# Performance work log

Hardware: AMD Instinct MI355X
Metric: run time of the kernel (lower is better)

## Reference

```python
import jax, jax.numpy as jnp
import numpy as np

N = 50000      # nodes
E = 800000     # edges
DIN = 128      # input_dim
FN = 128       # filter_num
OUT = 16       # out_dim (classes)
K = 10         # APPNP power-iteration steps
ALPHA = 0.1    # teleport probability


def _glorot_linear(key, fan_in, fan_out):
    s = 1.0 / np.sqrt(fan_in)
    kw, kb = jax.random.split(key)
    W = jax.random.uniform(kw, (fan_in, fan_out), jnp.float32, -s, s)
    b = jax.random.uniform(kb, (fan_out,), jnp.float32, -s, s)
    return W, b


def setup_inputs() -> dict:
    key = jax.random.key(0)
    ks = jax.random.split(key, 6)
    x = jax.random.normal(ks[0], (N, DIN), jnp.float32)
    edge_index = jax.random.randint(ks[1], (2, E), 0, N, dtype=jnp.int64)
    W1, b1 = _glorot_linear(ks[2], DIN, FN)
    W2, b2 = _glorot_linear(ks[3], FN, FN)
    W3, b3 = _glorot_linear(ks[4], FN, FN)
    Wc, bc = _glorot_linear(ks[5], FN, OUT)  # Conv1d kernel_size=1 == per-node linear
    return {"x": x, "edge_index": edge_index, "W1": W1, "b1": b1,
            "W2": W2, "b2": b2, "W3": W3, "b3": b3, "Wc": Wc, "bc": bc}


def _appnp(x, row, col, w, n):
    # x_{k+1} = (1-alpha) * A_hat @ x_k + alpha * x_0
    h = x
    def step(xk, _):
        msg = w[:, None] * xk[row]                      # [E+N, F] gather
        agg = jax.ops.segment_sum(msg, col, num_segments=n)  # scatter-add SpMM
        return (1.0 - ALPHA) * agg + ALPHA * h, None
    out, _ = jax.lax.scan(step, x, None, length=K)
    return out


def reference(x, edge_index, W1, b1, W2, b2, W3, b3, Wc, bc):
    n = x.shape[0]
    # gcn_norm with self-loops: w_e = deg(col)^-1/2 * deg(row)^-1/2
    loops = jnp.arange(n, dtype=edge_index.dtype)
    row = jnp.concatenate([edge_index[0], loops])
    col = jnp.concatenate([edge_index[1], loops])
    deg = jax.ops.segment_sum(jnp.ones_like(col, x.dtype), col, num_segments=n)
    dinv = jnp.where(deg > 0, jax.lax.rsqrt(deg), 0.0)
    w = dinv[row] * dinv[col]

    h = jax.nn.relu(_appnp(x @ W1 + b1, row, col, w, n))
    h = jax.nn.relu(_appnp(h @ W2 + b2, row, col, w, n))
    h = jax.nn.relu(_appnp(h @ W3 + b3, row, col, w, n))
    logits = h @ Wc + bc                                # 1x1 Conv1d == linear
    return jax.nn.log_softmax(logits, axis=1)
```

## Files before the change

kernel.cpp:

```cpp
#include <hip/hip_runtime.h>
#include <math.h>

#define FD 128
#define NOUT 16
#define ALPHA_F 0.1f

typedef short short8 __attribute__((ext_vector_type(8)));
typedef float f32x4 __attribute__((ext_vector_type(4)));

__device__ __forceinline__ float bflo(unsigned u) { return __uint_as_float(u << 16); }
__device__ __forceinline__ float bfhi(unsigned u) { return __uint_as_float(u & 0xffff0000u); }
__device__ __forceinline__ unsigned f2bf(float f) {
    unsigned u = __float_as_uint(f);
    u += 0x7fffu + ((u >> 16) & 1u);
    return u >> 16;
}
__device__ __forceinline__ unsigned pack2(float a, float b) {
    return f2bf(a) | (f2bf(b) << 16);
}


__global__ void count_kernel(const int* __restrict__ cols, int* __restrict__ cnt, int e) {
    int i = blockIdx.x * blockDim.x + threadIdx.x;
    if (i < e) atomicAdd(&cnt[cols[i]], 1);
}

__global__ void dinv_kernel(const int* __restrict__ cnt, float* __restrict__ dinv, int n) {
    int i = blockIdx.x * blockDim.x + threadIdx.x;
    if (i < n) dinv[i] = rsqrtf((float)(cnt[i] + 1));
}

__device__ __forceinline__ int padded(int cnt) { return (cnt + 8) & ~7; }

__global__ void scan_partial_kernel(const int* __restrict__ cnt, int* __restrict__ bsum, int n) {
    __shared__ int sh[256];
    int base = blockIdx.x * 1024 + threadIdx.x * 4;
    int s = 0;
    #pragma unroll
    for (int j = 0; j < 4; ++j) { int i = base + j; if (i < n) s += padded(cnt[i]); }
    sh[threadIdx.x] = s; __syncthreads();
    for (int d = 128; d > 0; d >>= 1) {
        if ((int)threadIdx.x < d) sh[threadIdx.x] += sh[threadIdx.x + d];
        __syncthreads();
    }
    if (threadIdx.x == 0) bsum[blockIdx.x] = sh[0];
}

__global__ void scan_base_kernel(int* __restrict__ bsum, int* __restrict__ off, int nb, int n) {
    if (threadIdx.x == 0 && blockIdx.x == 0) {
        int run = 0;
        for (int b = 0; b < nb; ++b) { int t = bsum[b]; bsum[b] = run; run += t; }
        off[n] = run;
    }
}

__global__ void scan_final_kernel(const int* __restrict__ cnt, const int* __restrict__ bsum,
                                  int* __restrict__ off, int* __restrict__ cur, int n) {
    __shared__ int sh[256];
    int t = threadIdx.x;
    int base_i = blockIdx.x * 1024 + t * 4;
    int v[4]; int s = 0;
    #pragma unroll
    for (int j = 0; j < 4; ++j) { int i = base_i + j; v[j] = (i < n) ? padded(cnt[i]) : 0; s += v[j]; }
    sh[t] = s; __syncthreads();
    for (int d = 1; d < 256; d <<= 1) {
        int x = (t >= d) ? sh[t - d] : 0;
        __syncthreads();
        sh[t] += x;
        __syncthreads();
    }
    int excl = sh[t] - s + bsum[blockIdx.x];
    #pragma unroll
    for (int j = 0; j < 4; ++j) {
        int i = base_i + j;
        if (i < n) { off[i] = excl; cur[i] = excl; }
        excl += v[j];
    }
}

__global__ void fill_edges_kernel(const int* __restrict__ rows, const int* __restrict__ cols,
                                  const float* __restrict__ dinv, int* __restrict__ cur,
                                  unsigned* __restrict__ eg, int e) {
    int i = blockIdx.x * blockDim.x + threadIdx.x;
    if (i < e) {
        int r = rows[i];
        int c = cols[i];
        int pos = atomicAdd(&cur[c], 1);
        eg[pos] = (f2bf(dinv[r] * dinv[c]) << 16) | (unsigned)r;
    }
}

__global__ void fill_loops_kernel(const float* __restrict__ dinv, int* __restrict__ cur,
                                  unsigned* __restrict__ eg, int n) {
    int i = blockIdx.x * blockDim.x + threadIdx.x;
    if (i < n) {
        int pos = atomicAdd(&cur[i], 1);
        eg[pos] = (f2bf(dinv[i] * dinv[i]) << 16) | (unsigned)i;
    }
}


__global__ void wtrans_kernel(const float* __restrict__ W, unsigned* __restrict__ Wt) {
    int idx = blockIdx.x * 256 + threadIdx.x;
    if (idx < 128 * 64) {
        int c = idx >> 6, ku = idx & 63;
        Wt[idx] = pack2(W[(2 * ku) * FD + c], W[(2 * ku + 1) * FD + c]);
    }
}

__global__ void xconv_kernel(const float* __restrict__ x, unsigned* __restrict__ Xb, int total) {
    int idx = blockIdx.x * blockDim.x + threadIdx.x;
    if (idx < total) {
        float2 f = ((const float2*)x)[idx];
        Xb[idx] = pack2(f.x, f.y);
    }
}

__global__ __launch_bounds__(256, 4)
void gemm_mfma_kernel(const unsigned* __restrict__ Xb, const unsigned* __restrict__ Wt,
                      const float* __restrict__ bias,
                      unsigned* __restrict__ Ab, unsigned* __restrict__ Z0b, int n) {
    int l = threadIdx.x & 63;
    int w = threadIdx.x >> 6;
    int l15 = l & 15, lq = l >> 4;
    int r0 = blockIdx.x * 64 + w * 16;
    int arow = min(r0 + l15, n - 1);
    const unsigned* aptr = Xb + (size_t)arow * 64 + lq * 4;
    const unsigned* bptr = Wt + (size_t)l15 * 64 + lq * 4;

    f32x4 acc[8];
    #pragma unroll
    for (int nt = 0; nt < 8; ++nt) acc[nt] = (f32x4){0.f, 0.f, 0.f, 0.f};

    #pragma unroll
    for (int kk = 0; kk < 4; ++kk) {
        short8 af = *(const short8*)(aptr + kk * 16);
        #pragma unroll
        for (int nt = 0; nt < 8; ++nt) {
            short8 bf = *(const short8*)(bptr + nt * 1024 + kk * 16);
            acc[nt] = __builtin_amdgcn_mfma_f32_16x16x32_bf16(af, bf, acc[nt], 0, 0, 0);
        }
    }

    #pragma unroll
    for (int nt = 0; nt < 8; ++nt) {
        float b_ = bias[nt * 16 + l15];
        #pragma unroll
        for (int j = 0; j < 4; ++j) {
            float v = acc[nt][j] + b_;
            float vp = __shfl_xor(v, 1);
            int row = r0 + lq * 4 + j;
            if (!(l & 1) && row < n) {
                int cu = nt * 8 + (l15 >> 1);
                Ab[(size_t)row * 64 + cu]  = pack2(v, vp);
                Z0b[(size_t)row * 64 + cu] = pack2(ALPHA_F * v, ALPHA_F * vp);
            }
        }
    }
}

__global__ __launch_bounds__(256, 8)
void spmm_bf16_kernel(const int* __restrict__ off, const unsigned* __restrict__ eg,
                      const unsigned* __restrict__ Xin, const unsigned* __restrict__ X0b,
                      unsigned* __restrict__ Xout, int n, int relu) {
    int node = blockIdx.x * 8 + ((int)threadIdx.x >> 5);
    if (node >= n) return;
    int lane31 = threadIdx.x & 31;
    int s = off[node];
    int degpad = off[node + 1] - s;
    int dother = __shfl_xor(degpad, 32);
    int dm = max(degpad, dother);
    const uint2* Xg = (const uint2*)Xin;
    uint2 x0 = ((const uint2*)X0b)[node * 32 + lane31];
    float a0 = 0.f, a1 = 0.f, a2 = 0.f, a3 = 0.f;

    for (int base = 0; base < dm; base += 8) {
        int p = s + min(base, degpad - 8);
        bool live = base < degpad;
        uint4 ra = *(const uint4*)(eg + p);
        uint4 rb = *(const uint4*)(eg + p + 4);
        uint2 g0 = Xg[(ra.x & 0xffffu) * 32 + lane31];
        uint2 g1 = Xg[(ra.y & 0xffffu) * 32 + lane31];
        uint2 g2 = Xg[(ra.z & 0xffffu) * 32 + lane31];
        uint2 g3 = Xg[(ra.w & 0xffffu) * 32 + lane31];
        uint2 g4 = Xg[(rb.x & 0xffffu) * 32 + lane31];
        uint2 g5 = Xg[(rb.y & 0xffffu) * 32 + lane31];
        uint2 g6 = Xg[(rb.z & 0xffffu) * 32 + lane31];
        uint2 g7 = Xg[(rb.w & 0xffffu) * 32 + lane31];
        float w0 = live ? bfhi(ra.x) : 0.f;
        float w1 = live ? bfhi(ra.y) : 0.f;
        float w2 = live ? bfhi(ra.z) : 0.f;
        float w3 = live ? bfhi(ra.w) : 0.f;
        float w4 = live ? bfhi(rb.x) : 0.f;
        float w5 = live ? bfhi(rb.y) : 0.f;
        float w6 = live ? bfhi(rb.z) : 0.f;
        float w7 = live ? bfhi(rb.w) : 0.f;
        a0 += w0 * bflo(g0.x); a1 += w0 * bfhi(g0.x); a2 += w0 * bflo(g0.y); a3 += w0 * bfhi(g0.y);
        a0 += w1 * bflo(g1.x); a1 += w1 * bfhi(g1.x); a2 += w1 * bflo(g1.y); a3 += w1 * bfhi(g1.y);
        a0 += w2 * bflo(g2.x); a1 += w2 * bfhi(g2.x); a2 += w2 * bflo(g2.y); a3 += w2 * bfhi(g2.y);
        a0 += w3 * bflo(g3.x); a1 += w3 * bfhi(g3.x); a2 += w3 * bflo(g3.y); a3 += w3 * bfhi(g3.y);
        a0 += w4 * bflo(g4.x); a1 += w4 * bfhi(g4.x); a2 += w4 * bflo(g4.y); a3 += w4 * bfhi(g4.y);
        a0 += w5 * bflo(g5.x); a1 += w5 * bfhi(g5.x); a2 += w5 * bflo(g5.y); a3 += w5 * bfhi(g5.y);
        a0 += w6 * bflo(g6.x); a1 += w6 * bfhi(g6.x); a2 += w6 * bflo(g6.y); a3 += w6 * bfhi(g6.y);
        a0 += w7 * bflo(g7.x); a1 += w7 * bfhi(g7.x); a2 += w7 * bflo(g7.y); a3 += w7 * bfhi(g7.y);
    }

    float v0 = 0.9f * a0 + bflo(x0.x);
    float v1 = 0.9f * a1 + bfhi(x0.x);
    float v2 = 0.9f * a2 + bflo(x0.y);
    float v3 = 0.9f * a3 + bfhi(x0.y);
    if (relu) {
        v0 = fmaxf(v0, 0.f); v1 = fmaxf(v1, 0.f);
        v2 = fmaxf(v2, 0.f); v3 = fmaxf(v3, 0.f);
    }
    ((uint2*)Xout)[node * 32 + lane31] = make_uint2(pack2(v0, v1), pack2(v2, v3));
}

__global__ void head_kernel(const unsigned* __restrict__ Hb, const float* __restrict__ Wc,
                            const float* __restrict__ bc, float* __restrict__ out, int n) {
    int t = threadIdx.x;
    int o = t & (NOUT - 1);
    int node = blockIdx.x * (256 / NOUT) + (t >> 4);
    if (node >= n) return;
    float acc = bc[o];
    const uint4* hrow = (const uint4*)(Hb + (size_t)node * 64);
    #pragma unroll 4
    for (int k4 = 0; k4 < 16; ++k4) {
        uint4 u = hrow[k4];
        int k = k4 * 8;
        acc += bflo(u.x) * Wc[(k + 0) * NOUT + o];
        acc += bfhi(u.x) * Wc[(k + 1) * NOUT + o];
        acc += bflo(u.y) * Wc[(k + 2) * NOUT + o];
        acc += bfhi(u.y) * Wc[(k + 3) * NOUT + o];
        acc += bflo(u.z) * Wc[(k + 4) * NOUT + o];
        acc += bfhi(u.z) * Wc[(k + 5) * NOUT + o];
        acc += bflo(u.w) * Wc[(k + 6) * NOUT + o];
        acc += bfhi(u.w) * Wc[(k + 7) * NOUT + o];
    }
    float m = acc;
    #pragma unroll
    for (int d = NOUT / 2; d > 0; d >>= 1) m = fmaxf(m, __shfl_xor(m, d, NOUT));
    float ex = __expf(acc - m);
    float s = ex;
    #pragma unroll
    for (int d = NOUT / 2; d > 0; d >>= 1) s += __shfl_xor(s, d, NOUT);
    out[node * NOUT + o] = acc - m - __logf(s);
}


static inline size_t align256(size_t x) { return (x + 255) & ~(size_t)255; }

extern "C" void kernel_launch(void* const* d_in, const int* in_sizes, int n_in,
                              void* d_out, int out_size, void* d_ws, size_t ws_size,
                              hipStream_t stream) {
    const float* x  = (const float*)d_in[0];
    const int*   ei = (const int*)d_in[1];
    const float* W1 = (const float*)d_in[2];
    const float* b1 = (const float*)d_in[3];
    const float* W2 = (const float*)d_in[4];
    const float* b2 = (const float*)d_in[5];
    const float* W3 = (const float*)d_in[6];
    const float* b3 = (const float*)d_in[7];
    const float* Wc = (const float*)d_in[8];
    const float* bc = (const float*)d_in[9];
    float* out = (float*)d_out;

    const int n = in_sizes[0] / FD;
    const int e = in_sizes[1] / 2;
    const int nnz_max = e + n + 8 * n + 16;
    const int nb = (n + 1023) / 1024;

    const int* rows = ei;
    const int* cols = ei + e;

    char* p = (char*)d_ws;
    int*      off  = (int*)p;       p += align256((size_t)(n + 1) * 4);
    int*      cur  = (int*)p;       p += align256((size_t)n * 4);
    float*    dinv = (float*)p;     p += align256((size_t)n * 4);
    int*      bsum = (int*)p;       p += align256((size_t)nb * 4);
    unsigned* eg   = (unsigned*)p;  p += align256((size_t)nnz_max * 4);
    unsigned* Wt   = (unsigned*)p;  p += align256((size_t)3 * 8192 * 4);
    unsigned* Ab   = (unsigned*)p;  p += align256((size_t)n * 64 * 4);
    unsigned* Bb   = (unsigned*)p;  p += align256((size_t)n * 64 * 4);
    unsigned* Z0b  = (unsigned*)p;  p += align256((size_t)n * 64 * 4);
    unsigned* Hb   = (unsigned*)p;  p += align256((size_t)n * 64 * 4);

    hipMemsetAsync(cur, 0, (size_t)n * 4, stream);
    hipMemsetAsync(eg, 0, (size_t)nnz_max * 4, stream);
    count_kernel<<<(e + 255) / 256, 256, 0, stream>>>(cols, cur, e);
    dinv_kernel<<<(n + 255) / 256, 256, 0, stream>>>(cur, dinv, n);
    scan_partial_kernel<<<nb, 256, 0, stream>>>(cur, bsum, n);
    scan_base_kernel<<<1, 64, 0, stream>>>(bsum, off, nb, n);
    scan_final_kernel<<<nb, 256, 0, stream>>>(cur, bsum, off, cur, n);
    fill_edges_kernel<<<(e + 255) / 256, 256, 0, stream>>>(rows, cols, dinv, cur, eg, e);
    fill_loops_kernel<<<(n + 255) / 256, 256, 0, stream>>>(dinv, cur, eg, n);

    wtrans_kernel<<<32, 256, 0, stream>>>(W1, Wt);
    wtrans_kernel<<<32, 256, 0, stream>>>(W2, Wt + 8192);
    wtrans_kernel<<<32, 256, 0, stream>>>(W3, Wt + 16384);
    xconv_kernel<<<(n * 64 + 255) / 256, 256, 0, stream>>>(x, Hb, n * 64);

    const int gemm_grid = (n + 63) / 64;
    const int spmm_grid = (n + 7) / 8;
    const float* bl[3] = { b1, b2, b3 };

    for (int st = 0; st < 3; ++st) {
        gemm_mfma_kernel<<<gemm_grid, 256, 0, stream>>>(Hb, Wt + st * 8192, bl[st], Ab, Z0b, n);
        unsigned* bufs[2] = { Ab, Bb };
        int cu = 0;
        for (int k = 0; k < 10; ++k) {
            unsigned* o_ = (k == 9) ? Hb : bufs[cu ^ 1];
            spmm_bf16_kernel<<<spmm_grid, 256, 0, stream>>>(off, eg, bufs[cu], Z0b, o_, n, k == 9);
            cu ^= 1;
        }
    }

    head_kernel<<<(n + 15) / 16, 256, 0, stream>>>(Hb, Wc, bc, out, n);
}
```

Before: 1.121 ms.

## Slice SpMM feature dimension across blocks and split edges across lane groups

Rewrites the APPNP propagation kernel so each block handles four nodes on one of four 32-feature slices. Each wave splits a node's edges across four 16-lane groups and combines them with cross-lane shuffle reductions. The aim is to keep the gathered slice of X resident in cache across the concurrently running blocks for the same slice, and to balance the work of low-degree nodes across more lanes. In exchange it issues smaller 4-byte gathers, reads the edge list four times, and adds shuffle reduction overhead. The tail handling assumes the padded degree is a multiple of 8.

```diff
diff --git a/kernel.cpp b/kernel.cpp
--- a/kernel.cpp
+++ b/kernel.cpp
@@ -160,60 +160,58 @@
 }
 
 __global__ __launch_bounds__(256, 8)
-void spmm_bf16_kernel(const int* __restrict__ off, const unsigned* __restrict__ eg,
-                      const unsigned* __restrict__ Xin, const unsigned* __restrict__ X0b,
-                      unsigned* __restrict__ Xout, int n, int relu) {
-    int node = blockIdx.x * 8 + ((int)threadIdx.x >> 5);
+void spmm_sliced_kernel(const int* __restrict__ off, const unsigned* __restrict__ eg,
+                        const unsigned* __restrict__ Xin, const unsigned* __restrict__ X0b,
+                        unsigned* __restrict__ Xout, int n, int relu) {
+    int b = blockIdx.x;
+    int s = b & 3;
+    int node = ((b >> 2) << 2) + ((int)threadIdx.x >> 6);
     if (node >= n) return;
-    int lane31 = threadIdx.x & 31;
-    int s = off[node];
-    int degpad = off[node + 1] - s;
-    int dother = __shfl_xor(degpad, 32);
-    int dm = max(degpad, dother);
-    const uint2* Xg = (const uint2*)Xin;
-    uint2 x0 = ((const uint2*)X0b)[node * 32 + lane31];
-    float a0 = 0.f, a1 = 0.f, a2 = 0.f, a3 = 0.f;
-
-    for (int base = 0; base < dm; base += 8) {
-        int p = s + min(base, degpad - 8);
-        bool live = base < degpad;
-        uint4 ra = *(const uint4*)(eg + p);
-        uint4 rb = *(const uint4*)(eg + p + 4);
-        uint2 g0 = Xg[(ra.x & 0xffffu) * 32 + lane31];
-        uint2 g1 = Xg[(ra.y & 0xffffu) * 32 + lane31];
-        uint2 g2 = Xg[(ra.z & 0xffffu) * 32 + lane31];
-        uint2 g3 = Xg[(ra.w & 0xffffu) * 32 + lane31];
-        uint2 g4 = Xg[(rb.x & 0xffffu) * 32 + lane31];
-        uint2 g5 = Xg[(rb.y & 0xffffu) * 32 + lane31];
-        uint2 g6 = Xg[(rb.z & 0xffffu) * 32 + lane31];
-        uint2 g7 = Xg[(rb.w & 0xffffu) * 32 + lane31];
-        float w0 = live ? bfhi(ra.x) : 0.f;
-        float w1 = live ? bfhi(ra.y) : 0.f;
-        float w2 = live ? bfhi(ra.z) : 0.f;
-        float w3 = live ? bfhi(ra.w) : 0.f;
-        float w4 = live ? bfhi(rb.x) : 0.f;
-        float w5 = live ? bfhi(rb.y) : 0.f;
-        float w6 = live ? bfhi(rb.z) : 0.f;
-        float w7 = live ? bfhi(rb.w) : 0.f;
-        a0 += w0 * bflo(g0.x); a1 += w0 * bfhi(g0.x); a2 += w0 * bflo(g0.y); a3 += w0 * bfhi(g0.y);
-        a0 += w1 * bflo(g1.x); a1 += w1 * bfhi(g1.x); a2 += w1 * bflo(g1.y); a3 += w1 * bfhi(g1.y);
-        a0 += w2 * bflo(g2.x); a1 += w2 * bfhi(g2.x); a2 += w2 * bflo(g2.y); a3 += w2 * bfhi(g2.y);
-        a0 += w3 * bflo(g3.x); a1 += w3 * bfhi(g3.x); a2 += w3 * bflo(g3.y); a3 += w3 * bfhi(g3.y);
-        a0 += w4 * bflo(g4.x); a1 += w4 * bfhi(g4.x); a2 += w4 * bflo(g4.y); a3 += w4 * bfhi(g4.y);
-        a0 += w5 * bflo(g5.x); a1 += w5 * bfhi(g5.x); a2 += w5 * bflo(g5.y); a3 += w5 * bfhi(g5.y);
-        a0 += w6 * bflo(g6.x); a1 += w6 * bfhi(g6.x); a2 += w6 * bflo(g6.y); a3 += w6 * bfhi(g6.y);
-        a0 += w7 * bflo(g7.x); a1 += w7 * bfhi(g7.x); a2 += w7 * bflo(g7.y); a3 += w7 * bfhi(g7.y);
-    }
-
-    float v0 = 0.9f * a0 + bflo(x0.x);
-    float v1 = 0.9f * a1 + bfhi(x0.x);
-    float v2 = 0.9f * a2 + bflo(x0.y);
-    float v3 = 0.9f * a3 + bfhi(x0.y);
-    if (relu) {
-        v0 = fmaxf(v0, 0.f); v1 = fmaxf(v1, 0.f);
-        v2 = fmaxf(v2, 0.f); v3 = fmaxf(v3, 0.f);
-    }
-    ((uint2*)Xout)[node * 32 + lane31] = make_uint2(pack2(v0, v1), pack2(v2, v3));
+    int l = threadIdx.x & 63;
+    int esub = l >> 4;
+    int fu = l & 15;
+    int p0 = off[node];
+    int deg = off[node + 1] - p0;
+    const unsigned* Xs = Xin + s * 16 + fu;
+    unsigned x0 = X0b[(size_t)node * 64 + s * 16 + fu];
+    const unsigned* ep = eg + p0 + esub;
+
+    float a0 = 0.f, a1 = 0.f;
+    int c = 0;
+    for (; c + 16 <= deg; c += 16) {
+        unsigned r0 = ep[c + 0];
+        unsigned r1 = ep[c + 4];
+        unsigned r2 = ep[c + 8];
+        unsigned r3 = ep[c + 12];
+        unsigned g0 = Xs[(r0 & 0xffffu) * 64u];
+        unsigned g1 = Xs[(r1 & 0xffffu) * 64u];
+        unsigned g2 = Xs[(r2 & 0xffffu) * 64u];
+        unsigned g3 = Xs[(r3 & 0xffffu) * 64u];
+        float w0 = bfhi(r0), w1 = bfhi(r1), w2 = bfhi(r2), w3 = bfhi(r3);
+        a0 += w0 * bflo(g0); a1 += w0 * bfhi(g0);
+        a0 += w1 * bflo(g1); a1 += w1 * bfhi(g1);
+        a0 += w2 * bflo(g2); a1 += w2 * bfhi(g2);
+        a0 += w3 * bflo(g3); a1 += w3 * bfhi(g3);
+    }
+    if (c < deg) {
+        unsigned r0 = ep[c + 0];
+        unsigned r1 = ep[c + 4];
+        unsigned g0 = Xs[(r0 & 0xffffu) * 64u];
+        unsigned g1 = Xs[(r1 & 0xffffu) * 64u];
+        float w0 = bfhi(r0), w1 = bfhi(r1);
+        a0 += w0 * bflo(g0); a1 += w0 * bfhi(g0);
+        a0 += w1 * bflo(g1); a1 += w1 * bfhi(g1);
+    }
+
+    a0 += __shfl_xor(a0, 16); a0 += __shfl_xor(a0, 32);
+    a1 += __shfl_xor(a1, 16); a1 += __shfl_xor(a1, 32);
+
+    if (esub == 0) {
+        float v0 = 0.9f * a0 + bflo(x0);
+        float v1 = 0.9f * a1 + bfhi(x0);
+        if (relu) { v0 = fmaxf(v0, 0.f); v1 = fmaxf(v1, 0.f); }
+        Xout[(size_t)node * 64 + s * 16 + fu] = pack2(v0, v1);
+    }
 }
 
 __global__ void head_kernel(const unsigned* __restrict__ Hb, const float* __restrict__ Wc,
@@ -301,7 +299,7 @@
     xconv_kernel<<<(n * 64 + 255) / 256, 256, 0, stream>>>(x, Hb, n * 64);
 
     const int gemm_grid = (n + 63) / 64;
-    const int spmm_grid = (n + 7) / 8;
+    const int spmm_grid = ((n + 3) / 4) * 4;
     const float* bl[3] = { b1, b2, b3 };
 
     for (int st = 0; st < 3; ++st) {
@@ -310,7 +308,7 @@
         int cu = 0;
         for (int k = 0; k < 10; ++k) {
             unsigned* o_ = (k == 9) ? Hb : bufs[cu ^ 1];
-            spmm_bf16_kernel<<<spmm_grid, 256, 0, stream>>>(off, eg, bufs[cu], Z0b, o_, n, k == 9);
+            spmm_sliced_kernel<<<spmm_grid, 256, 0, stream>>>(off, eg, bufs[cu], Z0b, o_, n, k == 9);
             cu ^= 1;
         }
     }
```

Result: slower. 1.942 ms (+73.3%).
